# Kernel tuning notes

Hardware: AMD Instinct MI355X
Metric: run time of the kernel (lower is better)

## Reference

```python
import jax, jax.numpy as jnp
import numpy as np
from jax import lax

N = 100_000      # active voxels
C = 64           # nIn == nOut
K = 343          # 7*7*7 depthwise taps
HID = 4 * C      # pointwise expansion
EPS = 1e-5
CENTER = K // 2  # self offset


def setup_inputs() -> dict:
    key = jax.random.key(0)
    ks = jax.random.split(key, 10)
    x_feat = jax.random.normal(ks[0], (N, C), dtype=jnp.float32)
    nbr = jax.random.randint(ks[1], (N, K), 0, N, dtype=jnp.int32)
    valid = jax.random.uniform(ks[2], (N, K)) < 0.25
    nbr = jnp.where(valid, nbr, jnp.int32(N))
    nbr = nbr.at[:, CENTER].set(jnp.arange(N, dtype=jnp.int32))  # submanifold: center is self
    W1 = jax.random.normal(ks[3], (K, C), dtype=jnp.float32) * 0.05
    b1 = jax.random.normal(ks[4], (C,), dtype=jnp.float32) * 0.02
    gamma = jnp.ones((C,), dtype=jnp.float32)
    beta = jnp.zeros((C,), dtype=jnp.float32)
    W2 = jax.random.normal(ks[5], (C, HID), dtype=jnp.float32) * (1.0 / np.sqrt(C))
    b2 = jax.random.normal(ks[6], (HID,), dtype=jnp.float32) * 0.02
    W3 = jax.random.normal(ks[7], (HID, C), dtype=jnp.float32) * (1.0 / np.sqrt(HID))
    b3 = jax.random.normal(ks[8], (C,), dtype=jnp.float32) * 0.02
    return {"x_feat": x_feat, "nbr_idx": nbr, "W1": W1, "b1": b1,
            "gamma": gamma, "beta": beta, "W2": W2, "b2": b2, "W3": W3, "b3": b3}


def _depthwise_submanifold(feat, nbr_idx, W1, b1):
    # feat [N,C]; nbr_idx [N,K] with sentinel N -> zero contribution
    feat_pad = jnp.concatenate([feat, jnp.zeros((1, feat.shape[1]), feat.dtype)], axis=0)
    def step(acc, xs):
        idx_k, w_k = xs                       # [N], [C]
        return acc + feat_pad[idx_k] * w_k, None  # gather + per-channel MAC
    acc0 = jnp.zeros_like(feat)
    out, _ = lax.scan(step, acc0, (nbr_idx.T, W1))  # scan over K=343 taps
    return out + b1


def _groupnorm1(h, gamma, beta):
    # num_groups=1 over channels, per active site
    mu = jnp.mean(h, axis=-1, keepdims=True)
    var = jnp.var(h, axis=-1, keepdims=True)
    return (h - mu) * lax.rsqrt(var + EPS) * gamma + beta


def reference(x_feat, nbr_idx, W1, b1, gamma, beta, W2, b2, W3, b3):
    h = _depthwise_submanifold(x_feat, nbr_idx, W1, b1)  # conv1 (depthwise 7^3)
    h = _groupnorm1(h, gamma, beta)                      # norm
    h = h @ W2 + b2                                      # conv2 (1x1x1, C->4C)
    h = jax.nn.gelu(h, approximate=False)                # exact GELU (torch default)
    h = h @ W3 + b3                                      # conv3 (1x1x1, 4C->C)
    return h + x_feat                                    # residual add
```

## Files before the change

### kernel.cpp

```cpp
#include <hip/hip_runtime.h>
#include <hip/hip_fp16.h>
#include <math.h>

#define CH    64
#define KT    343
#define HIDD  256
#define KCAP  144

typedef __attribute__((ext_vector_type(8))) _Float16 half8;
typedef __attribute__((ext_vector_type(4))) _Float16 half4;
typedef __attribute__((ext_vector_type(4))) float f32x4;
struct H24 { __half2 x, y, z, w; };

#define MEMBAR() asm volatile("" ::: "memory")

#define PRELOAD6(v, w)                                                     \
  { const int* row_ = nbr + (size_t)(w) * KT;                              \
    _Pragma("unroll") for (int p = 0; p < 6; ++p) {                        \
      const int tap_ = p * 64 + lane;                                      \
      v[p] = (tap_ < KT) ? row_[tap_] : N; } }

__global__ __launch_bounds__(256) void prep_compact_kernel(
    const float* __restrict__ W1, const float* __restrict__ W2,
    const float* __restrict__ W3, const float* __restrict__ x,
    const int* __restrict__ nbr, _Float16* __restrict__ W1h,
    _Float16* __restrict__ W2Th, _Float16* __restrict__ W3Th,
    _Float16* __restrict__ xh, int* __restrict__ packed,
    int* __restrict__ cnt, int N, int nelem) {
  const int t = blockIdx.x * 256 + threadIdx.x;
  const int step = gridDim.x * 256;
  for (int e = t; e < KT * CH; e += step) W1h[e] = (_Float16)W1[e];
  for (int e = t; e < CH * HIDD; e += step) {
    int k = e >> 8, n = e & 255;
    W2Th[n * CH + k] = (_Float16)W2[e];
  }
  for (int e = t; e < HIDD * CH; e += step) {
    int k = e >> 6, n = e & 63;
    W3Th[n * HIDD + k] = (_Float16)W3[e];
  }
  const int tot4 = nelem / 4 + 16;
  for (int q = t; q < tot4; q += step) {
    const int eb = q * 4;
    float4 v = (eb < nelem) ? *(const float4*)(x + eb) : make_float4(0.f, 0.f, 0.f, 0.f);
    half4 o;
    o[0] = (_Float16)v.x; o[1] = (_Float16)v.y;
    o[2] = (_Float16)v.z; o[3] = (_Float16)v.w;
    *(half4*)(xh + eb) = o;
  }

  const int lane = threadIdx.x & 63;
  const int wv = t >> 6;
  const int nw = (gridDim.x * 256) >> 6;
  int w = wv;
  if (w < N) {
    int v[6];
    PRELOAD6(v, w);
    while (w < N) {
      const int wn = w + nw;
      int vn[6];
      if (wn < N) PRELOAD6(vn, wn);
      int* prow = packed + (size_t)w * KCAP;
      int base = 0;
#pragma unroll
      for (int p = 0; p < 6; ++p) {
        const int tap = p * 64 + lane;
        const bool valid = (tap < KT) && (v[p] != N);
        const unsigned long long m = __ballot(valid);
        const int pos = __popcll(m & ((1ull << lane) - 1ull));
        if (valid) {
          const int wp = base + pos;
          if (wp < KCAP) prow[wp] = v[p] | (tap << 17);
        }
        base += __popcll(m);
      }
      if (lane == 0) cnt[w] = (base < KCAP) ? base : KCAP;
      w = wn;
#pragma unroll
      for (int p = 0; p < 6; ++p) v[p] = vn[p];
    }
  }
}

#define ISSUE8(buf, vi)                                                     \
  { _Pragma("unroll") for (int p = 0; p < 8; ++p) {                         \
      const int pk_ = __builtin_amdgcn_ds_bpermute(pb + 4 * p, (vi));       \
      buf[p] = *(const uint4*)(xb + ((((unsigned)pk_ & 0x1FFFFu) << 7) + (unsigned)e16)); } }

#define CONSUME8(buf, vi)                                                   \
  { _Pragma("unroll") for (int p = 0; p < 8; ++p) {                         \
      const int pk_ = __builtin_amdgcn_ds_bpermute(pb + 4 * p, (vi));       \
      const uint4 wq_ = *(const uint4*)&W1s[((((unsigned)pk_) >> 17) << 7) + e16]; \
      const H24 gh_ = __builtin_bit_cast(H24, buf[p]);                      \
      const H24 wh_ = __builtin_bit_cast(H24, wq_);                         \
      acc0 = __hfma2(gh_.x, wh_.x, acc0);                                   \
      acc1 = __hfma2(gh_.y, wh_.y, acc1);                                   \
      acc2 = __hfma2(gh_.z, wh_.z, acc2);                                   \
      acc3 = __hfma2(gh_.w, wh_.w, acc3); } }

__global__ __launch_bounds__(512, 2) void conv_kernel(
    const _Float16* __restrict__ xh, const int* __restrict__ packed,
    const int* __restrict__ cnt, const _Float16* __restrict__ W1h,
    const float* __restrict__ b1, const float* __restrict__ gamma,
    const float* __restrict__ beta, _Float16* __restrict__ h, int N) {
  __shared__ __align__(16) char W1s[43904];

  const int t = threadIdx.x;
  const int wvid = t >> 6;
  const int lane = t & 63;
  const int g = lane >> 3;
  const int e = lane & 7;
  const int e16 = e << 4;
  const int pb = (lane & 56) << 2;
  const int vbase = blockIdx.x * 64;
  const int vb = __builtin_amdgcn_readfirstlane(min(vbase + wvid * 8, N - 8));

  {
    const uint4* src = (const uint4*)W1h;
    uint4* dst = (uint4*)W1s;
    for (int q = t; q < 2744; q += 512) dst[q] = src[q];
  }

  const int cnt_g = cnt[vb + g];
  int mx = cnt_g;
  mx = max(mx, __shfl_xor(mx, 8));
  mx = max(mx, __shfl_xor(mx, 16));
  mx = max(mx, __shfl_xor(mx, 32));
  const int nck2 = __builtin_amdgcn_readfirstlane((((mx + 7) >> 3) + 1) & ~1);
  const int* prow = packed + (size_t)(vb + g) * KCAP;
  const int PADV = N;
  const char* xb = (const char*)xh;

  __half2 acc0 = __float2half2_rn(0.f), acc1 = acc0, acc2 = acc0, acc3 = acc0;

  uint4 ga[8], gb[8];

  #define LDE(ck) ( (((ck) * 8 + e) < cnt_g) ? prow[(ck) * 8 + e] : PADV )

  int viA = LDE(0);
  int viB = LDE(1);
  ISSUE8(ga, viA);
  __syncthreads();

  for (int ck = 0; ck < nck2; ck += 2) {
    const int viC = (ck + 2 < nck2) ? LDE(ck + 2) : PADV;
    MEMBAR();
    ISSUE8(gb, viB);
    MEMBAR();
    CONSUME8(ga, viA);
    const int viD = (ck + 3 < nck2) ? LDE(ck + 3) : PADV;
    MEMBAR();
    if (ck + 2 < nck2) ISSUE8(ga, viC);
    MEMBAR();
    CONSUME8(gb, viB);
    viA = viC;
    viB = viD;
  }

  float fa[8];
  fa[0] = __low2float(acc0); fa[1] = __high2float(acc0);
  fa[2] = __low2float(acc1); fa[3] = __high2float(acc1);
  fa[4] = __low2float(acc2); fa[5] = __high2float(acc2);
  fa[6] = __low2float(acc3); fa[7] = __high2float(acc3);
  {
    float4 blo = *(const float4*)(b1 + e * 8);
    float4 bhi = *(const float4*)(b1 + e * 8 + 4);
    fa[0] += blo.x; fa[1] += blo.y; fa[2] += blo.z; fa[3] += blo.w;
    fa[4] += bhi.x; fa[5] += bhi.y; fa[6] += bhi.z; fa[7] += bhi.w;
  }
  float s = 0.f, ss = 0.f;
#pragma unroll
  for (int d = 0; d < 8; ++d) { s += fa[d]; ss += fa[d] * fa[d]; }
  s += __shfl_xor(s, 1); ss += __shfl_xor(ss, 1);
  s += __shfl_xor(s, 2); ss += __shfl_xor(ss, 2);
  s += __shfl_xor(s, 4); ss += __shfl_xor(ss, 4);
  const float mu = s * (1.0f / 64.0f);
  const float var = ss * (1.0f / 64.0f) - mu * mu;
  const float inv = rsqrtf(var + 1e-5f);
  {
    float4 glo = *(const float4*)(gamma + e * 8);
    float4 ghi = *(const float4*)(gamma + e * 8 + 4);
    float4 tlo = *(const float4*)(beta + e * 8);
    float4 thi = *(const float4*)(beta + e * 8 + 4);
    const float gm[8] = {glo.x, glo.y, glo.z, glo.w, ghi.x, ghi.y, ghi.z, ghi.w};
    const float bt[8] = {tlo.x, tlo.y, tlo.z, tlo.w, thi.x, thi.y, thi.z, thi.w};
    half8 hv;
#pragma unroll
    for (int d = 0; d < 8; ++d)
      hv[d] = (_Float16)((fa[d] - mu) * inv * gm[d] + bt[d]);
    *(half8*)&h[(size_t)(vb + g) * CH + e * 8] = hv;
  }
}

__global__ __launch_bounds__(256, 2) void mlp_kernel(
    const _Float16* __restrict__ h, const float* __restrict__ x,
    const _Float16* __restrict__ W2Th, const float* __restrict__ b2,
    const _Float16* __restrict__ W3Th, const float* __restrict__ b3,
    float* __restrict__ out, int N) {
  __shared__ __align__(16) _Float16 gs[32][HIDD + 8];

  const int t = threadIdx.x;
  const int wvid = t >> 6;
  const int lane = t & 63;
  const int vbase = blockIdx.x * 32;
  const int row16 = lane & 15, quad = lane >> 4;

  half8 afr[2][2];
#pragma unroll
  for (int rt = 0; rt < 2; ++rt)
#pragma unroll
    for (int ks = 0; ks < 2; ++ks)
      afr[rt][ks] = *(const half8*)(h + (size_t)(vbase + rt * 16 + row16) * CH + ks * 32 + quad * 8);

#pragma unroll
  for (int cl = 0; cl < 4; ++cl) {
    const int n = wvid * 64 + cl * 16 + row16;
    f32x4 a0 = {0.f, 0.f, 0.f, 0.f}, a1 = {0.f, 0.f, 0.f, 0.f};
#pragma unroll
    for (int ks = 0; ks < 2; ++ks) {
      half8 bfr = *(const half8*)(W2Th + (size_t)n * CH + ks * 32 + quad * 8);
      a0 = __builtin_amdgcn_mfma_f32_16x16x32_f16(afr[0][ks], bfr, a0, 0, 0, 0);
      a1 = __builtin_amdgcn_mfma_f32_16x16x32_f16(afr[1][ks], bfr, a1, 0, 0, 0);
    }
    const float bias = b2[n];
#pragma unroll
    for (int r = 0; r < 4; ++r) {
      float z0 = a0[r] + bias;
      float z1 = a1[r] + bias;
      gs[quad * 4 + r][n]      = (_Float16)(0.5f * z0 * (1.0f + erff(z0 * 0.70710678118654752f)));
      gs[16 + quad * 4 + r][n] = (_Float16)(0.5f * z1 * (1.0f + erff(z1 * 0.70710678118654752f)));
    }
  }
  __syncthreads();

  f32x4 o0 = {0.f, 0.f, 0.f, 0.f}, o1 = {0.f, 0.f, 0.f, 0.f};
  const int oc = wvid * 16 + row16;
#pragma unroll
  for (int ks = 0; ks < 8; ++ks) {
    half8 bfr = *(const half8*)(W3Th + (size_t)oc * HIDD + ks * 32 + quad * 8);
    half8 a20 = *(const half8*)&gs[row16][ks * 32 + quad * 8];
    half8 a21 = *(const half8*)&gs[16 + row16][ks * 32 + quad * 8];
    o0 = __builtin_amdgcn_mfma_f32_16x16x32_f16(a20, bfr, o0, 0, 0, 0);
    o1 = __builtin_amdgcn_mfma_f32_16x16x32_f16(a21, bfr, o1, 0, 0, 0);
  }
  const float bias3 = b3[oc];
#pragma unroll
  for (int r = 0; r < 4; ++r) {
    size_t v0 = (size_t)vbase + quad * 4 + r;
    size_t v1 = (size_t)vbase + 16 + quad * 4 + r;
    out[v0 * CH + oc] = o0[r] + bias3 + x[v0 * CH + oc];
    out[v1 * CH + oc] = o1[r] + bias3 + x[v1 * CH + oc];
  }
}

extern "C" void kernel_launch(void* const* d_in, const int* in_sizes, int n_in,
                              void* d_out, int out_size, void* d_ws, size_t ws_size,
                              hipStream_t stream) {
  const float* x_feat = (const float*)d_in[0];
  const int*   nbr    = (const int*)d_in[1];
  const float* W1     = (const float*)d_in[2];
  const float* b1     = (const float*)d_in[3];
  const float* gamma  = (const float*)d_in[4];
  const float* beta   = (const float*)d_in[5];
  const float* W2     = (const float*)d_in[6];
  const float* b2     = (const float*)d_in[7];
  const float* W3     = (const float*)d_in[8];
  const float* b3     = (const float*)d_in[9];
  float* out = (float*)d_out;

  const int N = in_sizes[0] / CH;

  char* ws = (char*)d_ws;
  size_t off = 0;
  _Float16* xh = (_Float16*)(ws + off);
  off += (((size_t)(N + 1) * CH * 2) + 255) & ~(size_t)255;
  _Float16* W1h = (_Float16*)(ws + off);
  off += ((size_t)KT * CH * 2 + 255) & ~(size_t)255;
  _Float16* W2Th = (_Float16*)(ws + off);
  off += ((size_t)HIDD * CH * 2 + 255) & ~(size_t)255;
  _Float16* W3Th = (_Float16*)(ws + off);
  off += ((size_t)CH * HIDD * 2 + 255) & ~(size_t)255;
  int* packed = (int*)(ws + off);
  off += ((size_t)N * KCAP * 4 + 255) & ~(size_t)255;
  int* cnt = (int*)(ws + off);
  off += ((size_t)N * 4 + 255) & ~(size_t)255;
  _Float16* h = (_Float16*)(ws + off);
  off += ((size_t)N * CH * 2 + 255) & ~(size_t)255;

  hipLaunchKernelGGL(prep_compact_kernel, dim3(4096), dim3(256), 0, stream,
                     W1, W2, W3, x_feat, nbr, W1h, W2Th, W3Th, xh,
                     packed, cnt, N, N * CH);
  hipLaunchKernelGGL(conv_kernel, dim3((N + 63) / 64), dim3(512), 0, stream,
                     xh, packed, cnt, W1h, b1, gamma, beta, h, N);
  hipLaunchKernelGGL(mlp_kernel, dim3(N / 32), dim3(256), 0, stream,
                     h, x_feat, W2Th, b2, W3Th, b3, out, N);
}
```

Baseline: 422.8 us.

## Shrink conv LDS footprint with global fallback and smaller blocks; double-pipeline compaction

Only the first 316 depthwise taps are staged in LDS, and taps beyond that read weights from global memory. Blocks drop to 256 threads covering 32 voxels, so more blocks fit per CU. The compaction loop in the prep kernel now handles two voxel rows per wave per iteration to keep more neighbor loads in flight. The tap-dependent branch adds divergence and extra global traffic for high taps. The grid of N/32 blocks also assumes N is a multiple of 32, since the N-8 clamp was removed.

```diff
diff --git a/kernel.cpp b/kernel.cpp
--- a/kernel.cpp
+++ b/kernel.cpp
@@ -6,6 +6,7 @@
 #define KT    343
 #define HIDD  256
 #define KCAP  144
+#define LDS_TAPS 316
 
 typedef __attribute__((ext_vector_type(8))) _Float16 half8;
 typedef __attribute__((ext_vector_type(4))) _Float16 half4;
@@ -19,6 +20,22 @@
     _Pragma("unroll") for (int p = 0; p < 6; ++p) {                        \
       const int tap_ = p * 64 + lane;                                      \
       v[p] = (tap_ < KT) ? row_[tap_] : N; } }
+
+#define COMPACT1(w, v)                                                     \
+  { int* prow_ = packed + (size_t)(w) * KCAP;                              \
+    int base_ = 0;                                                         \
+    _Pragma("unroll") for (int p = 0; p < 6; ++p) {                        \
+      const int tap_ = p * 64 + lane;                                      \
+      const bool valid_ = (tap_ < KT) && (v[p] != N);                      \
+      const unsigned long long m_ = __ballot(valid_);                      \
+      const int pos_ = __popcll(m_ & ((1ull << lane) - 1ull));             \
+      if (valid_) {                                                        \
+        const int wp_ = base_ + pos_;                                      \
+        if (wp_ < KCAP) prow_[wp_] = v[p] | (tap_ << 17);                  \
+      }                                                                    \
+      base_ += __popcll(m_);                                               \
+    }                                                                      \
+    if (lane == 0) cnt[w] = (base_ < KCAP) ? base_ : KCAP; }
 
 __global__ __launch_bounds__(256) void prep_compact_kernel(
     const float* __restrict__ W1, const float* __restrict__ W2,
@@ -51,32 +68,23 @@
   const int lane = threadIdx.x & 63;
   const int wv = t >> 6;
   const int nw = (gridDim.x * 256) >> 6;
-  int w = wv;
-  if (w < N) {
-    int v[6];
-    PRELOAD6(v, w);
-    while (w < N) {
-      const int wn = w + nw;
-      int vn[6];
-      if (wn < N) PRELOAD6(vn, wn);
-      int* prow = packed + (size_t)w * KCAP;
-      int base = 0;
-#pragma unroll
-      for (int p = 0; p < 6; ++p) {
-        const int tap = p * 64 + lane;
-        const bool valid = (tap < KT) && (v[p] != N);
-        const unsigned long long m = __ballot(valid);
-        const int pos = __popcll(m & ((1ull << lane) - 1ull));
-        if (valid) {
-          const int wp = base + pos;
-          if (wp < KCAP) prow[wp] = v[p] | (tap << 17);
-        }
-        base += __popcll(m);
-      }
-      if (lane == 0) cnt[w] = (base < KCAP) ? base : KCAP;
-      w = wn;
-#pragma unroll
-      for (int p = 0; p < 6; ++p) v[p] = vn[p];
+  const int nw2 = nw * 2;
+  int wA = wv;
+  int wB = wv + nw;
+  if (wA < N) {
+    int vA[6], vB[6];
+    PRELOAD6(vA, wA);
+    if (wB < N) PRELOAD6(vB, wB);
+    while (wA < N) {
+      const int wA2 = wA + nw2, wB2 = wB + nw2;
+      int vnA[6], vnB[6];
+      if (wA2 < N) PRELOAD6(vnA, wA2);
+      if (wB2 < N) PRELOAD6(vnB, wB2);
+      COMPACT1(wA, vA);
+      if (wB < N) COMPACT1(wB, vB);
+      wA = wA2; wB = wB2;
+#pragma unroll
+      for (int p = 0; p < 6; ++p) { vA[p] = vnA[p]; vB[p] = vnB[p]; }
     }
   }
 }
@@ -89,7 +97,10 @@
 #define CONSUME8(buf, vi)                                                   \
   { _Pragma("unroll") for (int p = 0; p < 8; ++p) {                         \
       const int pk_ = __builtin_amdgcn_ds_bpermute(pb + 4 * p, (vi));       \
-      const uint4 wq_ = *(const uint4*)&W1s[((((unsigned)pk_) >> 17) << 7) + e16]; \
+      const unsigned tap_ = ((unsigned)pk_) >> 17;                          \
+      const uint4 wq_ = (tap_ < LDS_TAPS)                                   \
+          ? *(const uint4*)&W1s[(tap_ << 7) + e16]                          \
+          : *(const uint4*)(w1b + ((size_t)tap_ << 7) + (unsigned)e16);     \
       const H24 gh_ = __builtin_bit_cast(H24, buf[p]);                      \
       const H24 wh_ = __builtin_bit_cast(H24, wq_);                         \
       acc0 = __hfma2(gh_.x, wh_.x, acc0);                                   \
@@ -97,12 +108,12 @@
       acc2 = __hfma2(gh_.z, wh_.z, acc2);                                   \
       acc3 = __hfma2(gh_.w, wh_.w, acc3); } }
 
-__global__ __launch_bounds__(512, 2) void conv_kernel(
+__global__ __launch_bounds__(256, 3) void conv_kernel(
     const _Float16* __restrict__ xh, const int* __restrict__ packed,
     const int* __restrict__ cnt, const _Float16* __restrict__ W1h,
     const float* __restrict__ b1, const float* __restrict__ gamma,
     const float* __restrict__ beta, _Float16* __restrict__ h, int N) {
-  __shared__ __align__(16) char W1s[43904];
+  __shared__ __align__(16) char W1s[LDS_TAPS * 128];
 
   const int t = threadIdx.x;
   const int wvid = t >> 6;
@@ -111,13 +122,13 @@
   const int e = lane & 7;
   const int e16 = e << 4;
   const int pb = (lane & 56) << 2;
-  const int vbase = blockIdx.x * 64;
-  const int vb = __builtin_amdgcn_readfirstlane(min(vbase + wvid * 8, N - 8));
+  const int vbase = blockIdx.x * 32;
+  const int vb = __builtin_amdgcn_readfirstlane(vbase + wvid * 8);
 
   {
     const uint4* src = (const uint4*)W1h;
     uint4* dst = (uint4*)W1s;
-    for (int q = t; q < 2744; q += 512) dst[q] = src[q];
+    for (int q = t; q < LDS_TAPS * 8; q += 256) dst[q] = src[q];
   }
 
   const int cnt_g = cnt[vb + g];
@@ -129,6 +140,7 @@
   const int* prow = packed + (size_t)(vb + g) * KCAP;
   const int PADV = N;
   const char* xb = (const char*)xh;
+  const char* w1b = (const char*)W1h;
 
   __half2 acc0 = __float2half2_rn(0.f), acc1 = acc0, acc2 = acc0, acc3 = acc0;
 
@@ -289,7 +301,7 @@
   hipLaunchKernelGGL(prep_compact_kernel, dim3(4096), dim3(256), 0, stream,
                      W1, W2, W3, x_feat, nbr, W1h, W2Th, W3Th, xh,
                      packed, cnt, N, N * CH);
-  hipLaunchKernelGGL(conv_kernel, dim3((N + 63) / 64), dim3(512), 0, stream,
+  hipLaunchKernelGGL(conv_kernel, dim3(N / 32), dim3(256), 0, stream,
                      xh, packed, cnt, W1h, b1, gamma, beta, h, N);
   hipLaunchKernelGGL(mlp_kernel, dim3(N / 32), dim3(256), 0, stream,
                      h, x_feat, W2Th, b2, W3Th, b3, out, N);
```

Result: no change. 430.0 us (+1.7%).
